# Kernel tuning notes

Hardware: AMD Instinct MI355X
Metric: run time of the kernel (lower is better)

Reference implementation:

```python
import jax, jax.numpy as jnp
import numpy as np

N_NODES = 10000
N_EDGES = 640000
D_IN = 128
D_OUT = 128


def setup_inputs() -> dict:
    key = jax.random.key(0)
    k1, k2, k3, k4, k5 = jax.random.split(key, 5)
    feature = jax.random.normal(k1, (N_NODES, D_IN), dtype=jnp.float32)
    src = jax.random.randint(k2, (N_EDGES,), 0, N_NODES, dtype=jnp.int64)
    dst = jax.random.randint(k3, (N_EDGES,), 0, N_NODES, dtype=jnp.int64)
    W = jax.random.normal(k4, (D_IN, D_OUT), dtype=jnp.float32) / np.sqrt(D_IN)
    b = jax.random.normal(k5, (D_OUT,), dtype=jnp.float32) * 0.01
    return {"feature": feature, "src": src, "dst": dst, "W": W, "b": b}


def reference(feature, src, dst, W, b):
    # copy_u: gather source-node features onto edges, then sum into dst nodes
    msgs = feature[src]                                   # [E, D_IN]
    h = jax.ops.segment_sum(msgs, dst, num_segments=N_NODES)  # [N, D_IN]
    # dense linear
    return h @ W + b                                      # [N, D_OUT]
```

## Files before the change

### kernel.cpp

```cpp
#include <hip/hip_runtime.h>

constexpr int kNodes = 10000;
constexpr int kEdges = 640000;
constexpr int kD = 128;

typedef unsigned int   u32;
typedef unsigned short u16;

constexpr int kNB     = 625;
constexpr int kNCHUNK = 250;
constexpr int kCHUNK  = 2560;
constexpr int kCap    = 32;
constexpr int kRawMax = 1536;
constexpr int kGemmRows = 32;
constexpr int kGemmBlocks = (kNodes + kGemmRows - 1) / kGemmRows;

__device__ inline u16 f2bf(float x) {
    u32 u = __float_as_uint(x);
    u32 r = u + 0x7FFF + ((u >> 16) & 1);
    return (u16)(r >> 16);
}
__device__ inline float bf_lo(u32 v) { return __uint_as_float(v << 16); }
__device__ inline float bf_hi(u32 v) { return __uint_as_float(v & 0xFFFF0000u); }

__global__ void scatter_add_kernel(const float* __restrict__ feature,
                                   const int* __restrict__ src,
                                   const int* __restrict__ dst,
                                   float* __restrict__ h) {
    long long tid = (long long)blockIdx.x * blockDim.x + threadIdx.x;
    int e    = (int)(tid >> 5);
    int lane = (int)(tid & 31);
    if (e >= kEdges) return;
    int s = src[e];
    int d = dst[e];
    const float4 v = *reinterpret_cast<const float4*>(feature + (size_t)s * kD + lane * 4);
    float* hp = h + (size_t)d * kD + lane * 4;
    atomicAdd(hp + 0, v.x);
    atomicAdd(hp + 1, v.y);
    atomicAdd(hp + 2, v.z);
    atomicAdd(hp + 3, v.w);
}

__global__ __launch_bounds__(256)
void gemm_bias_kernel(const float* __restrict__ h,
                      const float* __restrict__ W,
                      const float* __restrict__ b,
                      float* __restrict__ out) {
    __shared__ float Wl[kD * kD];
    int t = threadIdx.x;
#pragma unroll
    for (int i = 0; i < 16; ++i) {
        int idx = t + i * 256;
        reinterpret_cast<float4*>(Wl)[idx] = reinterpret_cast<const float4*>(W)[idx];
    }
    __syncthreads();
    int row = blockIdx.x * 8 + (t >> 5);
    int j0  = (t & 31) * 4;
    if (row >= kNodes) return;
    const float* hrow = h + (size_t)row * kD;
    float4 acc = make_float4(0.f, 0.f, 0.f, 0.f);
#pragma unroll 4
    for (int k = 0; k < kD; k += 4) {
        float4 hv4 = *reinterpret_cast<const float4*>(hrow + k);
        const float* wk = Wl + (size_t)k * kD + j0;
        float4 w0 = *reinterpret_cast<const float4*>(wk + 0 * kD);
        float4 w1 = *reinterpret_cast<const float4*>(wk + 1 * kD);
        float4 w2 = *reinterpret_cast<const float4*>(wk + 2 * kD);
        float4 w3 = *reinterpret_cast<const float4*>(wk + 3 * kD);
        acc.x += hv4.x * w0.x + hv4.y * w1.x + hv4.z * w2.x + hv4.w * w3.x;
        acc.y += hv4.x * w0.y + hv4.y * w1.y + hv4.z * w2.y + hv4.w * w3.y;
        acc.z += hv4.x * w0.z + hv4.y * w1.z + hv4.z * w2.z + hv4.w * w3.z;
        acc.w += hv4.x * w0.w + hv4.y * w1.w + hv4.z * w2.w + hv4.w * w3.w;
    }
    const float4 bb = *reinterpret_cast<const float4*>(b + j0);
    acc.x += bb.x; acc.y += bb.y; acc.z += bb.z; acc.w += bb.w;
    *reinterpret_cast<float4*>(out + (size_t)row * kD + j0) = acc;
}

__global__ __launch_bounds__(256)
void phase1_kernel(const float* __restrict__ feature,
                   const float* __restrict__ W,
                   const int* __restrict__ src,
                   const int* __restrict__ dst,
                   u16* __restrict__ FW,
                   int* __restrict__ cnts,
                   u32* __restrict__ csr) {
    __shared__ float Wl[kD * kD];
    int t = threadIdx.x;

    if (blockIdx.x < kNCHUNK) {
        int* cur = reinterpret_cast<int*>(Wl);
        int blk  = blockIdx.x;

        for (int i = t; i < kNB; i += 256) cur[i] = 0;
        __syncthreads();

        int base = blk * kCHUNK;
        u32* myCsr = csr + (size_t)blk * kNB * kCap;
#pragma unroll
        for (int j = 0; j < 10; ++j) {
            int e = base + t + j * 256;
            int d = dst[e];
            int s = src[e];
            int bkt = d >> 4;
            int pos = atomicAdd(&cur[bkt], 1);
            if (pos < kCap)
                myCsr[bkt * kCap + pos] = ((u32)d << 16) | (u32)s;
        }
        __syncthreads();
        for (int i = t; i < kNB; i += 256) {
            int c = cur[i];
            cnts[blk * kNB + i] = c < kCap ? c : kCap;
        }
    } else {
#pragma unroll
        for (int i = 0; i < 16; ++i) {
            int idx = t + i * 256;
            reinterpret_cast<float4*>(Wl)[idx] = reinterpret_cast<const float4*>(W)[idx];
        }
        __syncthreads();

        int rp   = t >> 5;
        int j0   = (t & 31) * 4;
        int row0 = (blockIdx.x - kNCHUNK) * kGemmRows + rp * 4;
        int r0 = row0 + 0 < kNodes ? row0 + 0 : kNodes - 1;
        int r1 = row0 + 1 < kNodes ? row0 + 1 : kNodes - 1;
        int r2 = row0 + 2 < kNodes ? row0 + 2 : kNodes - 1;
        int r3 = row0 + 3 < kNodes ? row0 + 3 : kNodes - 1;
        const float* p0 = feature + (size_t)r0 * kD;
        const float* p1 = feature + (size_t)r1 * kD;
        const float* p2 = feature + (size_t)r2 * kD;
        const float* p3 = feature + (size_t)r3 * kD;

        float4 acc0 = make_float4(0.f, 0.f, 0.f, 0.f);
        float4 acc1 = make_float4(0.f, 0.f, 0.f, 0.f);
        float4 acc2 = make_float4(0.f, 0.f, 0.f, 0.f);
        float4 acc3 = make_float4(0.f, 0.f, 0.f, 0.f);
#pragma unroll 2
        for (int k = 0; k < kD; k += 4) {
            float4 a0 = *reinterpret_cast<const float4*>(p0 + k);
            float4 a1 = *reinterpret_cast<const float4*>(p1 + k);
            float4 a2 = *reinterpret_cast<const float4*>(p2 + k);
            float4 a3 = *reinterpret_cast<const float4*>(p3 + k);
            const float* wk = Wl + (size_t)k * kD + j0;
            float4 w0 = *reinterpret_cast<const float4*>(wk + 0 * kD);
            float4 w1 = *reinterpret_cast<const float4*>(wk + 1 * kD);
            float4 w2 = *reinterpret_cast<const float4*>(wk + 2 * kD);
            float4 w3 = *reinterpret_cast<const float4*>(wk + 3 * kD);
            acc0.x += a0.x * w0.x + a0.y * w1.x + a0.z * w2.x + a0.w * w3.x;
            acc0.y += a0.x * w0.y + a0.y * w1.y + a0.z * w2.y + a0.w * w3.y;
            acc0.z += a0.x * w0.z + a0.y * w1.z + a0.z * w2.z + a0.w * w3.z;
            acc0.w += a0.x * w0.w + a0.y * w1.w + a0.z * w2.w + a0.w * w3.w;
            acc1.x += a1.x * w0.x + a1.y * w1.x + a1.z * w2.x + a1.w * w3.x;
            acc1.y += a1.x * w0.y + a1.y * w1.y + a1.z * w2.y + a1.w * w3.y;
            acc1.z += a1.x * w0.z + a1.y * w1.z + a1.z * w2.z + a1.w * w3.z;
            acc1.w += a1.x * w0.w + a1.y * w1.w + a1.z * w2.w + a1.w * w3.w;
            acc2.x += a2.x * w0.x + a2.y * w1.x + a2.z * w2.x + a2.w * w3.x;
            acc2.y += a2.x * w0.y + a2.y * w1.y + a2.z * w2.y + a2.w * w3.y;
            acc2.z += a2.x * w0.z + a2.y * w1.z + a2.z * w2.z + a2.w * w3.z;
            acc2.w += a2.x * w0.w + a2.y * w1.w + a2.z * w2.w + a2.w * w3.w;
            acc3.x += a3.x * w0.x + a3.y * w1.x + a3.z * w2.x + a3.w * w3.x;
            acc3.y += a3.x * w0.y + a3.y * w1.y + a3.z * w2.y + a3.w * w3.y;
            acc3.z += a3.x * w0.z + a3.y * w1.z + a3.z * w2.z + a3.w * w3.z;
            acc3.w += a3.x * w0.w + a3.y * w1.w + a3.z * w2.w + a3.w * w3.w;
        }
        u32 lo, hi;
        if (row0 + 0 < kNodes) {
            lo = (u32)f2bf(acc0.x) | ((u32)f2bf(acc0.y) << 16);
            hi = (u32)f2bf(acc0.z) | ((u32)f2bf(acc0.w) << 16);
            *reinterpret_cast<uint2*>(FW + (size_t)(row0 + 0) * kD + j0) = make_uint2(lo, hi);
        }
        if (row0 + 1 < kNodes) {
            lo = (u32)f2bf(acc1.x) | ((u32)f2bf(acc1.y) << 16);
            hi = (u32)f2bf(acc1.z) | ((u32)f2bf(acc1.w) << 16);
            *reinterpret_cast<uint2*>(FW + (size_t)(row0 + 1) * kD + j0) = make_uint2(lo, hi);
        }
        if (row0 + 2 < kNodes) {
            lo = (u32)f2bf(acc2.x) | ((u32)f2bf(acc2.y) << 16);
            hi = (u32)f2bf(acc2.z) | ((u32)f2bf(acc2.w) << 16);
            *reinterpret_cast<uint2*>(FW + (size_t)(row0 + 2) * kD + j0) = make_uint2(lo, hi);
        }
        if (row0 + 3 < kNodes) {
            lo = (u32)f2bf(acc3.x) | ((u32)f2bf(acc3.y) << 16);
            hi = (u32)f2bf(acc3.z) | ((u32)f2bf(acc3.w) << 16);
            *reinterpret_cast<uint2*>(FW + (size_t)(row0 + 3) * kD + j0) = make_uint2(lo, hi);
        }
    }
}

__global__ __launch_bounds__(256)
void bucket_gather_kernel(const u16* __restrict__ FW,
                          const int* __restrict__ cnts,
                          const u32* __restrict__ csr,
                          const float* __restrict__ b,
                          float* __restrict__ out) {
    __shared__ u32 raw[kRawMax];
    __shared__ u16 srt[kRawMax];
    __shared__ int wtot[4], wbase[4];
    __shared__ int cnt16[16], noff16[16], cur16[16];
    int t   = threadIdx.x;
    int bkt = blockIdx.x;
    int wv   = t >> 6;
    int lane = t & 63;

    int myLen = (t < kNCHUNK) ? cnts[t * kNB + bkt] : 0;
    int incl = myLen;
#pragma unroll
    for (int off = 1; off < 64; off <<= 1) {
        int u = __shfl_up(incl, off);
        if (lane >= off) incl += u;
    }
    if (lane == 63) wtot[wv] = incl;
    if (t < 16) cnt16[t] = 0;
    __syncthreads();
    if (t == 0) {
        int r = 0;
#pragma unroll
        for (int i = 0; i < 4; ++i) { wbase[i] = r; r += wtot[i]; }
    }
    __syncthreads();
    int myBase = wbase[wv] + incl - myLen;
    int n = wbase[3] + wtot[3];
    if (n > kRawMax) n = kRawMax;

    if (myLen > 0) {
        const u32* sr = csr + ((size_t)t * kNB + bkt) * kCap;
        for (int i0 = 0; i0 < myLen; i0 += 4) {
            uint4 v4 = *reinterpret_cast<const uint4*>(sr + i0);
            int p = myBase + i0;
            if (p + 0 < kRawMax && i0 + 0 < myLen) raw[p + 0] = v4.x;
            if (p + 1 < kRawMax && i0 + 1 < myLen) raw[p + 1] = v4.y;
            if (p + 2 < kRawMax && i0 + 2 < myLen) raw[p + 2] = v4.z;
            if (p + 3 < kRawMax && i0 + 3 < myLen) raw[p + 3] = v4.w;
        }
    }
    __syncthreads();

    for (int i = t; i < n; i += 256) atomicAdd(&cnt16[(raw[i] >> 16) & 15], 1);
    __syncthreads();
    if (t == 0) {
        int r = 0;
#pragma unroll
        for (int i = 0; i < 16; ++i) { noff16[i] = r; cur16[i] = r; r += cnt16[i]; }
    }
    __syncthreads();
    for (int i = t; i < n; i += 256) {
        u32 r = raw[i];
        int p = atomicAdd(&cur16[(r >> 16) & 15], 1);
        srt[p] = (u16)(r & 0xFFFFu);
    }
    __syncthreads();

    int half   = lane >> 5;
    int lane32 = lane & 31;
    int nodeBase = bkt * 16;
    const float4 bb = *reinterpret_cast<const float4*>(b + lane32 * 4);

    for (int pr = wv; pr < 8; pr += 4) {
        int nd   = pr * 2 + half;
        int node = nodeBase + nd;
        int s0 = noff16[nd];
        int e0 = s0 + cnt16[nd];
        float ax = 0.f, ay = 0.f, az = 0.f, aw = 0.f;
        int i = s0;
        for (; i + 8 <= e0; i += 8) {
            uint2 v[8];
#pragma unroll
            for (int u = 0; u < 8; ++u) {
                int s = (int)srt[i + u];
                v[u] = *reinterpret_cast<const uint2*>(FW + (size_t)s * kD + lane32 * 4);
            }
#pragma unroll
            for (int u = 0; u < 8; ++u) {
                ax += bf_lo(v[u].x); ay += bf_hi(v[u].x);
                az += bf_lo(v[u].y); aw += bf_hi(v[u].y);
            }
        }
        for (; i < e0; ++i) {
            int s = (int)srt[i];
            uint2 v = *reinterpret_cast<const uint2*>(FW + (size_t)s * kD + lane32 * 4);
            ax += bf_lo(v.x); ay += bf_hi(v.x);
            az += bf_lo(v.y); aw += bf_hi(v.y);
        }
        *reinterpret_cast<float4*>(out + (size_t)node * kD + lane32 * 4) =
            make_float4(ax + bb.x, ay + bb.y, az + bb.z, aw + bb.w);
    }
}

extern "C" void kernel_launch(void* const* d_in, const int* in_sizes, int n_in,
                              void* d_out, int out_size, void* d_ws, size_t ws_size,
                              hipStream_t stream) {
    const float* feature = (const float*)d_in[0];
    const int*   src     = (const int*)d_in[1];
    const int*   dst     = (const int*)d_in[2];
    const float* W       = (const float*)d_in[3];
    const float* b       = (const float*)d_in[4];
    float*       out     = (float*)d_out;

    char* ws = (char*)d_ws;
    size_t off = 0;
    u16* FW   = (u16*)(ws + off);  off += (size_t)kNodes * kD * sizeof(u16);
    int* cnts = (int*)(ws + off);  off += (size_t)kNCHUNK * kNB * sizeof(int);
    off = (off + 127) & ~(size_t)127;
    u32* csr  = (u32*)(ws + off);  off += (size_t)kNCHUNK * kNB * kCap * sizeof(u32);
    const size_t neededB = off;
    const size_t neededA = (size_t)kNodes * kD * sizeof(float);

    if (ws_size >= neededB) {
        phase1_kernel<<<kNCHUNK + kGemmBlocks, 256, 0, stream>>>(
            feature, W, src, dst, FW, cnts, csr);
        bucket_gather_kernel<<<kNB, 256, 0, stream>>>(FW, cnts, csr, b, out);
    } else if (ws_size >= neededA) {
        float* h = (float*)d_ws;
        hipMemsetAsync(h, 0, neededA, stream);
        long long total = (long long)kEdges * 32;
        int threads = 256;
        int blocks  = (int)((total + threads - 1) / threads);
        scatter_add_kernel<<<blocks, threads, 0, stream>>>(feature, src, dst, h);
        gemm_bias_kernel<<<(kNodes + 7) / 8, 256, 0, stream>>>(h, W, b, out);
    }
}
```

Baseline: 45.49 us.

## Halve GEMM shared W tile and replace shuffle scan with shared-memory scan

Result: faster. 43.80 us (-3.7%).

```diff
diff --git a/kernel.cpp b/kernel.cpp
--- a/kernel.cpp
+++ b/kernel.cpp
@@ -12,7 +12,7 @@
 constexpr int kCHUNK  = 2560;
 constexpr int kCap    = 32;
 constexpr int kRawMax = 1536;
-constexpr int kGemmRows = 32;
+constexpr int kGemmRows   = 32;
 constexpr int kGemmBlocks = (kNodes + kGemmRows - 1) / kGemmRows;
 
 __device__ inline u16 f2bf(float x) {
@@ -85,7 +85,7 @@
                    u16* __restrict__ FW,
                    int* __restrict__ cnts,
                    u32* __restrict__ csr) {
-    __shared__ float Wl[kD * kD];
+    __shared__ float Wl[64 * kD];
     int t = threadIdx.x;
 
     if (blockIdx.x < kNCHUNK) {
@@ -113,13 +113,6 @@
             cnts[blk * kNB + i] = c < kCap ? c : kCap;
         }
     } else {
-#pragma unroll
-        for (int i = 0; i < 16; ++i) {
-            int idx = t + i * 256;
-            reinterpret_cast<float4*>(Wl)[idx] = reinterpret_cast<const float4*>(W)[idx];
-        }
-        __syncthreads();
-
         int rp   = t >> 5;
         int j0   = (t & 31) * 4;
         int row0 = (blockIdx.x - kNCHUNK) * kGemmRows + rp * 4;
@@ -136,34 +129,51 @@
         float4 acc1 = make_float4(0.f, 0.f, 0.f, 0.f);
         float4 acc2 = make_float4(0.f, 0.f, 0.f, 0.f);
         float4 acc3 = make_float4(0.f, 0.f, 0.f, 0.f);
-#pragma unroll 2
-        for (int k = 0; k < kD; k += 4) {
-            float4 a0 = *reinterpret_cast<const float4*>(p0 + k);
-            float4 a1 = *reinterpret_cast<const float4*>(p1 + k);
-            float4 a2 = *reinterpret_cast<const float4*>(p2 + k);
-            float4 a3 = *reinterpret_cast<const float4*>(p3 + k);
-            const float* wk = Wl + (size_t)k * kD + j0;
-            float4 w0 = *reinterpret_cast<const float4*>(wk + 0 * kD);
-            float4 w1 = *reinterpret_cast<const float4*>(wk + 1 * kD);
-            float4 w2 = *reinterpret_cast<const float4*>(wk + 2 * kD);
-            float4 w3 = *reinterpret_cast<const float4*>(wk + 3 * kD);
-            acc0.x += a0.x * w0.x + a0.y * w1.x + a0.z * w2.x + a0.w * w3.x;
-            acc0.y += a0.x * w0.y + a0.y * w1.y + a0.z * w2.y + a0.w * w3.y;
-            acc0.z += a0.x * w0.z + a0.y * w1.z + a0.z * w2.z + a0.w * w3.z;
-            acc0.w += a0.x * w0.w + a0.y * w1.w + a0.z * w2.w + a0.w * w3.w;
-            acc1.x += a1.x * w0.x + a1.y * w1.x + a1.z * w2.x + a1.w * w3.x;
-            acc1.y += a1.x * w0.y + a1.y * w1.y + a1.z * w2.y + a1.w * w3.y;
-            acc1.z += a1.x * w0.z + a1.y * w1.z + a1.z * w2.z + a1.w * w3.z;
-            acc1.w += a1.x * w0.w + a1.y * w1.w + a1.z * w2.w + a1.w * w3.w;
-            acc2.x += a2.x * w0.x + a2.y * w1.x + a2.z * w2.x + a2.w * w3.x;
-            acc2.y += a2.x * w0.y + a2.y * w1.y + a2.z * w2.y + a2.w * w3.y;
-            acc2.z += a2.x * w0.z + a2.y * w1.z + a2.z * w2.z + a2.w * w3.z;
-            acc2.w += a2.x * w0.w + a2.y * w1.w + a2.z * w2.w + a2.w * w3.w;
-            acc3.x += a3.x * w0.x + a3.y * w1.x + a3.z * w2.x + a3.w * w3.x;
-            acc3.y += a3.x * w0.y + a3.y * w1.y + a3.z * w2.y + a3.w * w3.y;
-            acc3.z += a3.x * w0.z + a3.y * w1.z + a3.z * w2.z + a3.w * w3.z;
-            acc3.w += a3.x * w0.w + a3.y * w1.w + a3.z * w2.w + a3.w * w3.w;
-        }
+
+        for (int kh = 0; kh < 2; ++kh) {
+            const float4* Wsrc = reinterpret_cast<const float4*>(W + (size_t)kh * 64 * kD);
+#pragma unroll
+            for (int i = 0; i < 8; ++i) {
+                int idx = t + i * 256;
+                reinterpret_cast<float4*>(Wl)[idx] = Wsrc[idx];
+            }
+            __syncthreads();
+
+            const float* ha0 = p0 + kh * 64;
+            const float* ha1 = p1 + kh * 64;
+            const float* ha2 = p2 + kh * 64;
+            const float* ha3 = p3 + kh * 64;
+#pragma unroll 4
+            for (int k = 0; k < 64; k += 4) {
+                float4 a0 = *reinterpret_cast<const float4*>(ha0 + k);
+                float4 a1 = *reinterpret_cast<const float4*>(ha1 + k);
+                float4 a2 = *reinterpret_cast<const float4*>(ha2 + k);
+                float4 a3 = *reinterpret_cast<const float4*>(ha3 + k);
+                const float* wk = Wl + (size_t)k * kD + j0;
+                float4 w0 = *reinterpret_cast<const float4*>(wk + 0 * kD);
+                float4 w1 = *reinterpret_cast<const float4*>(wk + 1 * kD);
+                float4 w2 = *reinterpret_cast<const float4*>(wk + 2 * kD);
+                float4 w3 = *reinterpret_cast<const float4*>(wk + 3 * kD);
+                acc0.x += a0.x * w0.x + a0.y * w1.x + a0.z * w2.x + a0.w * w3.x;
+                acc0.y += a0.x * w0.y + a0.y * w1.y + a0.z * w2.y + a0.w * w3.y;
+                acc0.z += a0.x * w0.z + a0.y * w1.z + a0.z * w2.z + a0.w * w3.z;
+                acc0.w += a0.x * w0.w + a0.y * w1.w + a0.z * w2.w + a0.w * w3.w;
+                acc1.x += a1.x * w0.x + a1.y * w1.x + a1.z * w2.x + a1.w * w3.x;
+                acc1.y += a1.x * w0.y + a1.y * w1.y + a1.z * w2.y + a1.w * w3.y;
+                acc1.z += a1.x * w0.z + a1.y * w1.z + a1.z * w2.z + a1.w * w3.z;
+                acc1.w += a1.x * w0.w + a1.y * w1.w + a1.z * w2.w + a1.w * w3.w;
+                acc2.x += a2.x * w0.x + a2.y * w1.x + a2.z * w2.x + a2.w * w3.x;
+                acc2.y += a2.x * w0.y + a2.y * w1.y + a2.z * w2.y + a2.w * w3.y;
+                acc2.z += a2.x * w0.z + a2.y * w1.z + a2.z * w2.z + a2.w * w3.z;
+                acc2.w += a2.x * w0.w + a2.y * w1.w + a2.z * w2.w + a2.w * w3.w;
+                acc3.x += a3.x * w0.x + a3.y * w1.x + a3.z * w2.x + a3.w * w3.x;
+                acc3.y += a3.x * w0.y + a3.y * w1.y + a3.z * w2.y + a3.w * w3.y;
+                acc3.z += a3.x * w0.z + a3.y * w1.z + a3.z * w2.z + a3.w * w3.z;
+                acc3.w += a3.x * w0.w + a3.y * w1.w + a3.z * w2.w + a3.w * w3.w;
+            }
+            if (kh == 0) __syncthreads();
+        }
+
         u32 lo, hi;
         if (row0 + 0 < kNodes) {
             lo = (u32)f2bf(acc0.x) | ((u32)f2bf(acc0.y) << 16);
@@ -196,31 +206,24 @@
                           float* __restrict__ out) {
     __shared__ u32 raw[kRawMax];
     __shared__ u16 srt[kRawMax];
-    __shared__ int wtot[4], wbase[4];
+    __shared__ int ps[256];
     __shared__ int cnt16[16], noff16[16], cur16[16];
     int t   = threadIdx.x;
     int bkt = blockIdx.x;
-    int wv   = t >> 6;
-    int lane = t & 63;
 
     int myLen = (t < kNCHUNK) ? cnts[t * kNB + bkt] : 0;
-    int incl = myLen;
-#pragma unroll
-    for (int off = 1; off < 64; off <<= 1) {
-        int u = __shfl_up(incl, off);
-        if (lane >= off) incl += u;
-    }
-    if (lane == 63) wtot[wv] = incl;
+    ps[t] = myLen;
+    __syncthreads();
+    for (int off = 1; off < 256; off <<= 1) {
+        int add = (t >= off) ? ps[t - off] : 0;
+        __syncthreads();
+        ps[t] += add;
+        __syncthreads();
+    }
+    int myBase = ps[t] - myLen;
     if (t < 16) cnt16[t] = 0;
     __syncthreads();
-    if (t == 0) {
-        int r = 0;
-#pragma unroll
-        for (int i = 0; i < 4; ++i) { wbase[i] = r; r += wtot[i]; }
-    }
-    __syncthreads();
-    int myBase = wbase[wv] + incl - myLen;
-    int n = wbase[3] + wtot[3];
+    int n = ps[255];
     if (n > kRawMax) n = kRawMax;
 
     if (myLen > 0) {
@@ -251,6 +254,8 @@
     }
     __syncthreads();
 
+    int wv     = t >> 6;
+    int lane   = t & 63;
     int half   = lane >> 5;
     int lane32 = lane & 31;
     int nodeBase = bkt * 16;
```
